# Kernel optimization log

Hardware: AMD Instinct MI355X
Metric: run time of the kernel (lower is better)

Reference implementation:

```python
import jax, jax.numpy as jnp
import numpy as np

N, E, D, H, C = 100000, 1600000, 128, 128, 47
EPS = 1e-5


def setup_inputs() -> dict:
    key = jax.random.key(0)
    ks = jax.random.split(key, 10)
    s = 1.0 / np.sqrt(D).astype(np.float32)
    return {
        "x": jax.random.normal(ks[0], (N, D), jnp.float32),
        "edge_index": jax.random.randint(ks[1], (2, E), 0, N, jnp.int32),
        "Wl0": jax.random.normal(ks[2], (H, D), jnp.float32) * s,
        "bl0": jnp.zeros((H,), jnp.float32),
        "Wr0": jax.random.normal(ks[3], (H, D), jnp.float32) * s,
        "g0": jnp.ones((H,), jnp.float32),
        "b0": jnp.zeros((H,), jnp.float32),
        "Wl1": jax.random.normal(ks[4], (H, H), jnp.float32) * s,
        "bl1": jnp.zeros((H,), jnp.float32),
        "Wr1": jax.random.normal(ks[5], (H, H), jnp.float32) * s,
        "g1": jnp.ones((H,), jnp.float32),
        "b1": jnp.zeros((H,), jnp.float32),
        "Wl2": jax.random.normal(ks[6], (C, H), jnp.float32) * s,
        "bl2": jnp.zeros((C,), jnp.float32),
        "Wr2": jax.random.normal(ks[7], (C, H), jnp.float32) * s,
    }


def _sage_conv(x, edge_index, Wl, bl, Wr):
    # PyG SAGEConv(mean aggr): out = lin_l(mean_{j in N(i)} x_j) + lin_r(x_i)
    dst, src = edge_index[0], edge_index[1]
    n = x.shape[0]
    msg = x[src]                                             # [E, d] gather
    summed = jax.ops.segment_sum(msg, dst, num_segments=n)   # [N, d] scatter-add
    deg = jax.ops.segment_sum(jnp.ones((msg.shape[0],), x.dtype), dst, num_segments=n)
    agg = summed / jnp.maximum(deg, 1.0)[:, None]            # mean over neighbors
    return agg @ Wl.T + bl + x @ Wr.T


def _bn(x, g, b):
    # BatchNorm1d, training-mode batch statistics (biased variance)
    mu = jnp.mean(x, axis=0)
    var = jnp.mean(jnp.square(x - mu), axis=0)
    return (x - mu) * jax.lax.rsqrt(var + EPS) * g + b


def reference(x, edge_index, Wl0, bl0, Wr0, g0, b0, Wl1, bl1, Wr1, g1, b1, Wl2, bl2, Wr2):
    h = _sage_conv(x, edge_index, Wl0, bl0, Wr0)
    h = jax.nn.relu(_bn(h, g0, b0))          # dropout treated as identity (deterministic reference)
    h = _sage_conv(h, edge_index, Wl1, bl1, Wr1)
    h = jax.nn.relu(_bn(h, g1, b1))
    return _sage_conv(h, edge_index, Wl2, bl2, Wr2)
```

## Files before the change

### kernel.cpp

```cpp
#include <hip/hip_runtime.h>

typedef __attribute__((ext_vector_type(8))) short short8;
typedef __attribute__((ext_vector_type(4))) float f32x4;

constexpr float BN_EPS = 1e-5f;
#define NBUCKETS 128
#define SLOT 24576

__device__ __forceinline__ ushort f2bf(float f) {
  uint u = __float_as_uint(f);
  u = (u + 0x7fffu + ((u >> 16) & 1u)) >> 16;
  return (ushort)u;
}
__device__ __forceinline__ float bf2f(ushort h) { return __uint_as_float((uint)h << 16); }
__device__ __forceinline__ float bf2f_lo(uint v) { return __uint_as_float(v << 16); }
__device__ __forceinline__ float bf2f_hi(uint v) { return __uint_as_float(v & 0xffff0000u); }

typedef __attribute__((address_space(1))) const unsigned int* as1_cu32;
typedef __attribute__((address_space(3))) unsigned int* as3_u32;
__device__ __forceinline__ void gload_lds16(const void* g, void* l) {
  __builtin_amdgcn_global_load_lds((as1_cu32)g, (as3_u32)l, 16, 0, 0);
}


__global__ __launch_bounds__(256) void k_prep(const int* __restrict__ dst, const int* __restrict__ src, int E,
                                              int* __restrict__ bcur, uint* __restrict__ ebuf,
                                              const float* __restrict__ x, ushort* __restrict__ Xb, int n4,
                                              const float* __restrict__ Wl0, const float* __restrict__ Wr0,
                                              const float* __restrict__ Wl1, const float* __restrict__ Wr1,
                                              const float* __restrict__ Wl2, const float* __restrict__ Wr2,
                                              ushort* __restrict__ W0l, ushort* __restrict__ W0r,
                                              ushort* __restrict__ W1l, ushort* __restrict__ W1r,
                                              ushort* __restrict__ Wc, float* __restrict__ statsAll,
                                              int C, int binGrid, int castGrid) {
  int bb = blockIdx.x;
  if (bb < binGrid) {
    __shared__ int h[NBUCKETS];
    __shared__ int base[NBUCKETS];
    __shared__ int cur[NBUCKETS];
    const int e0 = bb * 8192;
    const int e1 = min(e0 + 8192, E);
    for (int i = threadIdx.x; i < NBUCKETS; i += 256) h[i] = 0;
    __syncthreads();
    for (int e = e0 + threadIdx.x * 4; e < e1; e += 1024) {
      int4 d = *reinterpret_cast<const int4*>(&dst[e]);
      if (e + 3 < e1) {
        atomicAdd(&h[d.x >> 10], 1); atomicAdd(&h[d.y >> 10], 1);
        atomicAdd(&h[d.z >> 10], 1); atomicAdd(&h[d.w >> 10], 1);
      } else {
        for (int j = 0; e + j < e1; ++j) atomicAdd(&h[dst[e + j] >> 10], 1);
      }
    }
    __syncthreads();
    if (threadIdx.x < NBUCKETS) {
      base[threadIdx.x] = threadIdx.x * SLOT + atomicAdd(&bcur[threadIdx.x], h[threadIdx.x]);
      cur[threadIdx.x] = 0;
    }
    __syncthreads();
    for (int e = e0 + threadIdx.x * 4; e < e1; e += 1024) {
      int4 d = *reinterpret_cast<const int4*>(&dst[e]);
      int4 s = *reinterpret_cast<const int4*>(&src[e]);
      int dd[4] = {d.x, d.y, d.z, d.w};
      int ss[4] = {s.x, s.y, s.z, s.w};
      for (int j = 0; j < 4 && e + j < e1; ++j) {
        int b = dd[j] >> 10;
        int pos = base[b] + atomicAdd(&cur[b], 1);
        ebuf[pos] = (uint)(dd[j] & 1023) | ((uint)ss[j] << 10);
      }
    }
    return;
  }
  bb -= binGrid;
  if (bb < 64) {
    const float* s = (bb < 16) ? Wl0 : (bb < 32) ? Wr0 : (bb < 48) ? Wl1 : Wr1;
    ushort* d = (bb < 16) ? W0l : (bb < 32) ? W0r : (bb < 48) ? W1l : W1r;
    int i = (bb & 15) * 256 + threadIdx.x;
    float4 v = reinterpret_cast<const float4*>(s)[i];
    ushort4 o;
    o.x = f2bf(v.x); o.y = f2bf(v.y); o.z = f2bf(v.z); o.w = f2bf(v.w);
    reinterpret_cast<ushort4*>(d)[i] = o;
    return;
  }
  bb -= 64;
  if (bb < 64) {
    int i = bb * 256 + threadIdx.x;
    int r = i >> 7, k = i & 127;
    float v = 0.f;
    if (r < C) v = Wl2[r * 128 + k];
    else if (r >= 64 && r < 64 + C) v = Wr2[(r - 64) * 128 + k];
    Wc[i] = f2bf(v);
    return;
  }
  bb -= 64;
  if (bb < castGrid) {
    for (int i = bb * 256 + threadIdx.x; i < n4; i += castGrid * 256) {
      float4 v = reinterpret_cast<const float4*>(x)[i];
      ushort4 o;
      o.x = f2bf(v.x); o.y = f2bf(v.y); o.z = f2bf(v.z); o.w = f2bf(v.w);
      reinterpret_cast<ushort4*>(Xb)[i] = o;
    }
    return;
  }
  for (int i = threadIdx.x; i < 512; i += 256) statsAll[i] = 0.f;
}

__global__ __launch_bounds__(512) void k_bucket_build(const uint* __restrict__ ebuf, const int* __restrict__ bend,
                                                      int* __restrict__ rp, int* __restrict__ deg,
                                                      float* __restrict__ deg_inv, int* __restrict__ csr, int N) {
  __shared__ int cnt[1024];
  __shared__ int pre[1024];
  __shared__ int tmp[1024];
  const int blk = blockIdx.x, tid = threadIdx.x;
  const int base = blk << 10;
  const int p0 = blk * SLOT, p1 = p0 + bend[blk];
  for (int i = tid; i < 1024; i += 512) cnt[i] = 0;
  __syncthreads();
  for (int p = p0 + tid; p < p1; p += 512) atomicAdd(&cnt[ebuf[p] & 1023u], 1);
  __syncthreads();
  for (int i = tid; i < 1024; i += 512) pre[i] = cnt[i];
  __syncthreads();
  for (int off = 1; off < 1024; off <<= 1) {
    for (int i = tid; i < 1024; i += 512) tmp[i] = (i >= off) ? pre[i - off] : 0;
    __syncthreads();
    for (int i = tid; i < 1024; i += 512) pre[i] += tmp[i];
    __syncthreads();
  }
  for (int i = tid; i < 1024; i += 512) {
    int node = base + i;
    if (node < N) {
      int c = cnt[i];
      rp[node] = p0 + pre[i] - c;
      deg[node] = c;
      deg_inv[node] = 1.0f / (float)max(c, 1);
    }
    tmp[i] = pre[i] - cnt[i];
  }
  __syncthreads();
  for (int p = p0 + tid; p < p1; p += 512) {
    uint pr = ebuf[p];
    int pos = p0 + atomicAdd(&tmp[pr & 1023u], 1);
    csr[pos] = (int)(pr >> 10);
  }
}


template <bool PRE_BN>
__global__ __launch_bounds__(512, 4) void k_fused(const ushort* __restrict__ X, const ushort* __restrict__ Bsrc,
                                                  const ushort* __restrict__ WA, const ushort* __restrict__ WB,
                                                  const int* __restrict__ rp, const int* __restrict__ deg,
                                                  const float* __restrict__ deg_inv, const int* __restrict__ csr,
                                                  const float* __restrict__ sums, const float* __restrict__ gw,
                                                  const float* __restrict__ bw, float invM,
                                                  float* __restrict__ partial, ushort* __restrict__ Z, int M) {
  __shared__ ushort sA[64 * 128];
  __shared__ ushort sB[64 * 128];
  __shared__ float red[2][4][128];
  __shared__ float ssc[PRE_BN ? 128 : 1];
  __shared__ float ssh[PRE_BN ? 128 : 1];
  const int tid = threadIdx.x;
  const int wave = tid >> 6, lane = tid & 63;
  const int rfrag = lane & 15, kgrp = lane >> 4;
  const int li = rfrag;
  const int row0 = blockIdx.x * 64;

  if (PRE_BN && tid < 128) {
    float mean = sums[tid] * invM;
    float var = fmaxf(sums[128 + tid] * invM - mean * mean, 0.f);
    float sc = gw[tid] * rsqrtf(var + BN_EPS);
    ssc[tid] = sc;
    ssh[tid] = fmaf(-mean, sc, bw[tid]);
  }

#pragma unroll
  for (int i = 0; i < 2; ++i) {
    int c = wave * 2 + i;
    int lb = c * 1024 + lane * 16;
    int row = lb >> 8, bin = lb & 255;
    int gr = min(row0 + row, M - 1);
    int sb = bin ^ ((row & 7) << 4);
    gload_lds16((const char*)Bsrc + (size_t)gr * 256 + sb, (char*)sB + c * 1024);
  }

  float scr[8], shr[8];
  if (PRE_BN) {
#pragma unroll
    for (int e = 0; e < 8; ++e) {
      int f = li * 8 + e;
      float mean = sums[f] * invM;
      float var = fmaxf(sums[128 + f] * invM - mean * mean, 0.f);
      scr[e] = gw[f] * rsqrtf(var + BN_EPS);
      shr[e] = fmaf(-mean, scr[e], bw[f]);
    }
  }

#define BN8(vv, A0, A1, e0)                                                     \
  {                                                                             \
    float xl = bf2f_lo(vv), xh = bf2f_hi(vv);                                   \
    if (PRE_BN) {                                                               \
      xl = fmaxf(fmaf(xl, scr[e0], shr[e0]), 0.f);                              \
      xh = fmaxf(fmaf(xh, scr[e0 + 1], shr[e0 + 1]), 0.f);                      \
    }                                                                           \
    A0 += xl; A1 += xh;                                                         \
  }

  const uint4* X16 = reinterpret_cast<const uint4*>(X);
#pragma unroll
  for (int g = 0; g < 2; ++g) {
    const int lrow = wave * 8 + g * 4 + kgrp;
    const int node = row0 + lrow;
    float a0 = 0.f, a1 = 0.f, a2 = 0.f, a3 = 0.f, a4 = 0.f, a5 = 0.f, a6 = 0.f, a7 = 0.f;
    if (node < M) {
      const int start = rp[node];
      const int c = deg[node];
      int p = 0;
      for (; p + 7 < c; p += 8) {
        int idx[8];
#pragma unroll
        for (int u = 0; u < 8; ++u) idx[u] = csr[start + p + u];
        uint4 v[8];
#pragma unroll
        for (int u = 0; u < 8; ++u) v[u] = X16[(size_t)idx[u] * 16 + li];
#pragma unroll
        for (int u = 0; u < 8; ++u) {
          BN8(v[u].x, a0, a1, 0); BN8(v[u].y, a2, a3, 2);
          BN8(v[u].z, a4, a5, 4); BN8(v[u].w, a6, a7, 6);
        }
      }
      if (p + 3 < c) {
        int idx[4];
#pragma unroll
        for (int u = 0; u < 4; ++u) idx[u] = csr[start + p + u];
        uint4 v[4];
#pragma unroll
        for (int u = 0; u < 4; ++u) v[u] = X16[(size_t)idx[u] * 16 + li];
#pragma unroll
        for (int u = 0; u < 4; ++u) {
          BN8(v[u].x, a0, a1, 0); BN8(v[u].y, a2, a3, 2);
          BN8(v[u].z, a4, a5, 4); BN8(v[u].w, a6, a7, 6);
        }
        p += 4;
      }
      for (; p < c; ++p) {
        uint4 v = X16[(size_t)csr[start + p] * 16 + li];
        BN8(v.x, a0, a1, 0); BN8(v.y, a2, a3, 2);
        BN8(v.z, a4, a5, 4); BN8(v.w, a6, a7, 6);
      }
      const float di = deg_inv[node];
      a0 *= di; a1 *= di; a2 *= di; a3 *= di;
      a4 *= di; a5 *= di; a6 *= di; a7 *= di;
    }
    uint4 o;
    o.x = (uint)f2bf(a0) | ((uint)f2bf(a1) << 16);
    o.y = (uint)f2bf(a2) | ((uint)f2bf(a3) << 16);
    o.z = (uint)f2bf(a4) | ((uint)f2bf(a5) << 16);
    o.w = (uint)f2bf(a6) | ((uint)f2bf(a7) << 16);
    *reinterpret_cast<uint4*>((char*)sA + lrow * 256 + ((li * 16) ^ ((lrow & 7) << 4))) = o;
  }
#undef BN8

  short8 wfA[4], wfB[4];
  {
    const ushort* wa = WA + (wave * 16 + rfrag) * 128 + kgrp * 8;
    const ushort* wb = WB + (wave * 16 + rfrag) * 128 + kgrp * 8;
#pragma unroll
    for (int s = 0; s < 4; ++s) {
      wfA[s] = *reinterpret_cast<const short8*>(wa + s * 32);
      wfB[s] = *reinterpret_cast<const short8*>(wb + s * 32);
    }
  }
  __syncthreads();

  if (PRE_BN) {
#pragma unroll
    for (int i = 0; i < 2; ++i) {
      int addr = (wave * 2 + i) * 1024 + lane * 16;
      int row = addr >> 8, bin = addr & 255;
      int col0 = (bin ^ ((row & 7) << 4)) >> 1;
      uint4 v = *reinterpret_cast<const uint4*>((const char*)sB + addr);
      uint vv[4] = {v.x, v.y, v.z, v.w};
      uint ov[4];
#pragma unroll
      for (int q = 0; q < 4; ++q) {
        int f = col0 + q * 2;
        float xl = fmaxf(fmaf(bf2f_lo(vv[q]), ssc[f], ssh[f]), 0.f);
        float xh = fmaxf(fmaf(bf2f_hi(vv[q]), ssc[f + 1], ssh[f + 1]), 0.f);
        ov[q] = (uint)f2bf(xl) | ((uint)f2bf(xh) << 16);
      }
      *reinterpret_cast<uint4*>((char*)sB + addr) = make_uint4(ov[0], ov[1], ov[2], ov[3]);
    }
    __syncthreads();
  }

  f32x4 acc[4];
#pragma unroll
  for (int i = 0; i < 4; ++i) acc[i] = (f32x4){0.f, 0.f, 0.f, 0.f};

  const int rs = (rfrag & 7) << 4;
#pragma unroll
  for (int strip = 0; strip < 4; ++strip) {
    const int r = strip * 16 + rfrag;
    short8 af[4], bf[4];
#pragma unroll
    for (int s = 0; s < 4; ++s) {
      int off = (kgrp * 16 + s * 64) ^ rs;
      af[s] = *reinterpret_cast<const short8*>((const char*)sA + r * 256 + off);
      bf[s] = *reinterpret_cast<const short8*>((const char*)sB + r * 256 + off);
    }
#pragma unroll
    for (int s = 0; s < 4; ++s)
      acc[strip] = __builtin_amdgcn_mfma_f32_16x16x32_bf16(af[s], wfA[s], acc[strip], 0, 0, 0);
#pragma unroll
    for (int s = 0; s < 4; ++s)
      acc[strip] = __builtin_amdgcn_mfma_f32_16x16x32_bf16(bf[s], wfB[s], acc[strip], 0, 0, 0);
  }

  {
    float s1 = 0.f, s2 = 0.f;
#pragma unroll
    for (int strip = 0; strip < 4; ++strip) {
#pragma unroll
      for (int rr = 0; rr < 4; ++rr) {
        int grow = row0 + strip * 16 + kgrp * 4 + rr;
        if (grow < M) {
          float v = acc[strip][rr];
          s1 += v;
          s2 = fmaf(v, v, s2);
        }
      }
    }
    s1 += __shfl_xor(s1, 16); s2 += __shfl_xor(s2, 16);
    s1 += __shfl_xor(s1, 32); s2 += __shfl_xor(s2, 32);
    if (kgrp == 0) {
      partial[(size_t)blockIdx.x * 256 + wave * 16 + rfrag] = s1;
      partial[(size_t)blockIdx.x * 256 + 128 + wave * 16 + rfrag] = s2;
    }
  }
  __syncthreads();

  const int cb = (wave * 16 + rfrag) * 2;
#pragma unroll
  for (int strip = 0; strip < 4; ++strip) {
#pragma unroll
    for (int rr = 0; rr < 4; ++rr) {
      int row = strip * 16 + kgrp * 4 + rr;
      *reinterpret_cast<ushort*>((char*)sA + row * 256 + (cb ^ ((row & 7) << 4))) = f2bf(acc[strip][rr]);
    }
  }
  __syncthreads();

#pragma unroll
  for (int i = 0; i < 2; ++i) {
    int lb = (wave * 2 + i) * 1024 + lane * 16;
    int row = lb >> 8, bin = lb & 255;
    int gr = row0 + row;
    if (gr < M)
      *reinterpret_cast<uint4*>((char*)Z + (size_t)gr * 256 + bin) =
          *reinterpret_cast<const uint4*>((const char*)sA + row * 256 + (bin ^ ((row & 7) << 4)));
  }
}


__global__ __launch_bounds__(256) void k_bn_reduce(const float* __restrict__ partial, int nblk,
                                                   float* __restrict__ stats) {
  float acc = 0.f;
  for (int b = blockIdx.x; b < nblk; b += gridDim.x) acc += partial[(size_t)b * 256 + threadIdx.x];
  atomicAdd(&stats[threadIdx.x], acc);
}


__global__ __launch_bounds__(512, 6) void k_gemm1(const ushort* __restrict__ H, const ushort* __restrict__ Wc,
                                                  const float* __restrict__ sums, const float* __restrict__ gw,
                                                  const float* __restrict__ bw, float invM,
                                                  ushort* __restrict__ Yb, ushort* __restrict__ Rb, int M) {
  __shared__ ushort sA[64 * 128];
  __shared__ float ssc[128];
  __shared__ float ssh[128];
  const int tid = threadIdx.x;
  const int wave = tid >> 6, lane = tid & 63;
  const int rfrag = lane & 15, kgrp = lane >> 4;
  const int row0 = blockIdx.x * 64;

  if (tid < 128) {
    float mean = sums[tid] * invM;
    float var = fmaxf(sums[128 + tid] * invM - mean * mean, 0.f);
    float sc = gw[tid] * rsqrtf(var + BN_EPS);
    ssc[tid] = sc;
    ssh[tid] = fmaf(-mean, sc, bw[tid]);
  }

#pragma unroll
  for (int i = 0; i < 2; ++i) {
    int c = wave * 2 + i;
    int lb = c * 1024 + lane * 16;
    int row = lb >> 8, bin = lb & 255;
    int gr = min(row0 + row, M - 1);
    int sb = bin ^ ((row & 7) << 4);
    gload_lds16((const char*)H + (size_t)gr * 256 + sb, (char*)sA + c * 1024);
  }

  short8 wf[4];
  {
    const ushort* wp = Wc + (wave * 16 + rfrag) * 128 + kgrp * 8;
#pragma unroll
    for (int s = 0; s < 4; ++s) wf[s] = *reinterpret_cast<const short8*>(wp + s * 32);
  }
  __syncthreads();

#pragma unroll
  for (int i = 0; i < 2; ++i) {
    int addr = (wave * 2 + i) * 1024 + lane * 16;
    int row = addr >> 8, bin = addr & 255;
    int col0 = (bin ^ ((row & 7) << 4)) >> 1;
    uint4 v = *reinterpret_cast<const uint4*>((const char*)sA + addr);
    uint vv[4] = {v.x, v.y, v.z, v.w};
    uint ov[4];
#pragma unroll
    for (int q = 0; q < 4; ++q) {
      int f = col0 + q * 2;
      float xl = fmaxf(fmaf(bf2f_lo(vv[q]), ssc[f], ssh[f]), 0.f);
      float xh = fmaxf(fmaf(bf2f_hi(vv[q]), ssc[f + 1], ssh[f + 1]), 0.f);
      ov[q] = (uint)f2bf(xl) | ((uint)f2bf(xh) << 16);
    }
    *reinterpret_cast<uint4*>((char*)sA + addr) = make_uint4(ov[0], ov[1], ov[2], ov[3]);
  }
  __syncthreads();

  f32x4 acc[4];
#pragma unroll
  for (int i = 0; i < 4; ++i) acc[i] = (f32x4){0.f, 0.f, 0.f, 0.f};
  const int rs = (rfrag & 7) << 4;
#pragma unroll
  for (int strip = 0; strip < 4; ++strip) {
    const int r = strip * 16 + rfrag;
    short8 af[4];
#pragma unroll
    for (int s = 0; s < 4; ++s)
      af[s] = *reinterpret_cast<const short8*>((const char*)sA + r * 256 + ((kgrp * 16 + s * 64) ^ rs));
#pragma unroll
    for (int s = 0; s < 4; ++s)
      acc[strip] = __builtin_amdgcn_mfma_f32_16x16x32_bf16(af[s], wf[s], acc[strip], 0, 0, 0);
  }
  __syncthreads();

  const int cb = (wave * 16 + rfrag) * 2;
#pragma unroll
  for (int strip = 0; strip < 4; ++strip) {
#pragma unroll
    for (int rr = 0; rr < 4; ++rr) {
      int row = strip * 16 + kgrp * 4 + rr;
      *reinterpret_cast<ushort*>((char*)sA + row * 256 + (cb ^ ((row & 7) << 4))) = f2bf(acc[strip][rr]);
    }
  }
  __syncthreads();

#pragma unroll
  for (int i = 0; i < 2; ++i) {
    int lb = (wave * 2 + i) * 1024 + lane * 16;
    int row = lb >> 8, bin = lb & 255;
    int gr = row0 + row;
    if (gr < M) {
      uint4 v = *reinterpret_cast<const uint4*>((const char*)sA + row * 256 + (bin ^ ((row & 7) << 4)));
      if (bin < 128) *reinterpret_cast<uint4*>((char*)Yb + (size_t)gr * 128 + bin) = v;
      else *reinterpret_cast<uint4*>((char*)Rb + (size_t)gr * 128 + (bin - 128)) = v;
    }
  }
}


__global__ __launch_bounds__(256) void k_agg47(const ushort* __restrict__ Yb, const ushort* __restrict__ Rb,
                                               const float* __restrict__ bias, const int* __restrict__ rp,
                                               const int* __restrict__ deg, const float* __restrict__ deg_inv,
                                               const int* __restrict__ csr, float* __restrict__ out,
                                               int N, int C) {
  const int wave = threadIdx.x >> 6, lane = threadIdx.x & 63;
  const int sub = lane >> 3, li = lane & 7;
  const int node = blockIdx.x * 32 + wave * 8 + sub;
  if (node >= N) return;
  const int start = rp[node];
  const int c = deg[node];
  const uint4* Y16 = reinterpret_cast<const uint4*>(Yb);
  float a0 = 0.f, a1 = 0.f, a2 = 0.f, a3 = 0.f, a4 = 0.f, a5 = 0.f, a6 = 0.f, a7 = 0.f;
  int p = 0;
  for (; p + 7 < c; p += 8) {
    int idx[8];
#pragma unroll
    for (int u = 0; u < 8; ++u) idx[u] = csr[start + p + u];
    uint4 v[8];
#pragma unroll
    for (int u = 0; u < 8; ++u) v[u] = Y16[(size_t)idx[u] * 8 + li];
#pragma unroll
    for (int u = 0; u < 8; ++u) {
      a0 += bf2f_lo(v[u].x); a1 += bf2f_hi(v[u].x);
      a2 += bf2f_lo(v[u].y); a3 += bf2f_hi(v[u].y);
      a4 += bf2f_lo(v[u].z); a5 += bf2f_hi(v[u].z);
      a6 += bf2f_lo(v[u].w); a7 += bf2f_hi(v[u].w);
    }
  }
  for (; p < c; ++p) {
    uint4 v = Y16[(size_t)csr[start + p] * 8 + li];
    a0 += bf2f_lo(v.x); a1 += bf2f_hi(v.x);
    a2 += bf2f_lo(v.y); a3 += bf2f_hi(v.y);
    a4 += bf2f_lo(v.z); a5 += bf2f_hi(v.z);
    a6 += bf2f_lo(v.w); a7 += bf2f_hi(v.w);
  }
  const float di = deg_inv[node];
  uint4 sv = reinterpret_cast<const uint4*>(Rb)[(size_t)node * 8 + li];
  float s[8] = {bf2f_lo(sv.x), bf2f_hi(sv.x), bf2f_lo(sv.y), bf2f_hi(sv.y),
                bf2f_lo(sv.z), bf2f_hi(sv.z), bf2f_lo(sv.w), bf2f_hi(sv.w)};
  float a[8] = {a0, a1, a2, a3, a4, a5, a6, a7};
#pragma unroll
  for (int j = 0; j < 8; ++j) {
    int f = li * 8 + j;
    if (f < C) out[(size_t)node * C + f] = fmaf(a[j], di, s[j] + bias[f]);
  }
}


extern "C" void kernel_launch(void* const* d_in, const int* in_sizes, int n_in,
                              void* d_out, int out_size, void* d_ws, size_t ws_size,
                              hipStream_t stream) {
  const float* x   = (const float*)d_in[0];
  const int*   ei  = (const int*)d_in[1];
  const float* Wl0 = (const float*)d_in[2];
  const float* Wr0 = (const float*)d_in[4];
  const float* g0  = (const float*)d_in[5];
  const float* b0  = (const float*)d_in[6];
  const float* Wl1 = (const float*)d_in[7];
  const float* Wr1 = (const float*)d_in[9];
  const float* g1  = (const float*)d_in[10];
  const float* b1  = (const float*)d_in[11];
  const float* Wl2 = (const float*)d_in[12];
  const float* bl2 = (const float*)d_in[13];
  const float* Wr2 = (const float*)d_in[14];

  const int N = in_sizes[0] / 128;
  const int E = in_sizes[1] / 2;
  const int C = in_sizes[13];

  const int* edst = ei;
  const int* esrc = ei + E;

  char* w = (char*)d_ws;
  auto al = [](size_t v) { return (v + 255) & ~(size_t)255; };
  size_t off = 0;
  int*    bcur    = (int*)(w + off);    off = al(off + NBUCKETS * 4);
  float*  stats   = (float*)(w + off);  off = al(off + 512 * 4);
  int*    rp      = (int*)(w + off);    off = al(off + (size_t)N * 4);
  int*    deg     = (int*)(w + off);    off = al(off + (size_t)N * 4);
  float*  deg_inv = (float*)(w + off);  off = al(off + (size_t)N * 4);
  int*    csr     = (int*)(w + off);    off = al(off + (size_t)NBUCKETS * SLOT * 4);
  uint*   ebuf    = (uint*)(w + off);   off = al(off + (size_t)NBUCKETS * SLOT * 4);
  ushort* Xb      = (ushort*)(w + off); off = al(off + (size_t)N * 128 * 2);
  ushort* hA      = (ushort*)(w + off); off = al(off + (size_t)N * 128 * 2);
  ushort* hB      = (ushort*)(w + off); off = al(off + (size_t)N * 128 * 2);
  ushort* W0l     = (ushort*)(w + off); off = al(off + 16384 * 2);
  ushort* W0r     = (ushort*)(w + off); off = al(off + 16384 * 2);
  ushort* W1l     = (ushort*)(w + off); off = al(off + 16384 * 2);
  ushort* W1r     = (ushort*)(w + off); off = al(off + 16384 * 2);
  ushort* Wc      = (ushort*)(w + off); off = al(off + 16384 * 2);
  const int nblkG = (N + 63) / 64;
  float*  partial = (float*)(w + off);  off = al(off + (size_t)nblkG * 256 * 4);

  float* stats0 = stats;
  float* stats1 = stats + 256;
  ushort* Yb = hB;
  ushort* Rb = hB + (size_t)N * 64;

  const int binGrid = (E + 8191) / 8192;
  const int castGrid = 384;
  const int nbBuck = (N + 1023) / 1024;
  const int agg47Grid = (N + 31) / 32;
  const float invM = 1.0f / (float)N;

  hipMemsetAsync(bcur, 0, NBUCKETS * 4, stream);

  k_prep<<<binGrid + 128 + castGrid + 1, 256, 0, stream>>>(
      edst, esrc, E, bcur, ebuf, x, Xb, N * 32,
      Wl0, Wr0, Wl1, Wr1, Wl2, Wr2, W0l, W0r, W1l, W1r, Wc, stats, C, binGrid, castGrid);

  k_bucket_build<<<nbBuck, 512, 0, stream>>>(ebuf, bcur, rp, deg, deg_inv, csr, N);

  k_fused<false><<<nblkG, 512, 0, stream>>>(Xb, Xb, W0l, W0r, rp, deg, deg_inv, csr,
                                            nullptr, nullptr, nullptr, 0.f, partial, hB, N);
  k_bn_reduce<<<64, 256, 0, stream>>>(partial, nblkG, stats0);

  k_fused<true><<<nblkG, 512, 0, stream>>>(hB, hB, W1l, W1r, rp, deg, deg_inv, csr,
                                           stats0, g0, b0, invM, partial, hA, N);
  k_bn_reduce<<<64, 256, 0, stream>>>(partial, nblkG, stats1);

  k_gemm1<<<nblkG, 512, 0, stream>>>(hA, Wc, stats1, g1, b1, invM, Yb, Rb, N);
  k_agg47<<<agg47Grid, 256, 0, stream>>>(Yb, Rb, bl2, rp, deg, deg_inv, csr, (float*)d_out, N, C);
}
```

Measured before the change: 344.4 us.

## Apply layer-0 BN+ReLU once in a standalone pass instead of per gathered neighbor

Layer 1 used to apply BN+ReLU to every gathered neighbor row inside the mean-aggregation loop, which repeats that work about once per incoming edge. This change adds a separate elementwise kernel that normalizes the layer-0 output in place, so a single non-templated fused kernel can do a plain gather-sum for both layers. It also prefetches the next eight CSR indices while the current neighbor rows are being accumulated. The cost is an extra kernel launch and a full read and write of the hidden activations. BN output is also now rounded to bf16 before aggregation, which slightly changes numerics.

```diff
diff --git a/kernel.cpp b/kernel.cpp
--- a/kernel.cpp
+++ b/kernel.cpp
@@ -144,32 +144,18 @@
 }
 
 
-template <bool PRE_BN>
 __global__ __launch_bounds__(512, 4) void k_fused(const ushort* __restrict__ X, const ushort* __restrict__ Bsrc,
                                                   const ushort* __restrict__ WA, const ushort* __restrict__ WB,
                                                   const int* __restrict__ rp, const int* __restrict__ deg,
                                                   const float* __restrict__ deg_inv, const int* __restrict__ csr,
-                                                  const float* __restrict__ sums, const float* __restrict__ gw,
-                                                  const float* __restrict__ bw, float invM,
                                                   float* __restrict__ partial, ushort* __restrict__ Z, int M) {
   __shared__ ushort sA[64 * 128];
   __shared__ ushort sB[64 * 128];
-  __shared__ float red[2][4][128];
-  __shared__ float ssc[PRE_BN ? 128 : 1];
-  __shared__ float ssh[PRE_BN ? 128 : 1];
   const int tid = threadIdx.x;
   const int wave = tid >> 6, lane = tid & 63;
   const int rfrag = lane & 15, kgrp = lane >> 4;
   const int li = rfrag;
   const int row0 = blockIdx.x * 64;
-
-  if (PRE_BN && tid < 128) {
-    float mean = sums[tid] * invM;
-    float var = fmaxf(sums[128 + tid] * invM - mean * mean, 0.f);
-    float sc = gw[tid] * rsqrtf(var + BN_EPS);
-    ssc[tid] = sc;
-    ssh[tid] = fmaf(-mean, sc, bw[tid]);
-  }
 
 #pragma unroll
   for (int i = 0; i < 2; ++i) {
@@ -179,28 +165,6 @@
     int gr = min(row0 + row, M - 1);
     int sb = bin ^ ((row & 7) << 4);
     gload_lds16((const char*)Bsrc + (size_t)gr * 256 + sb, (char*)sB + c * 1024);
-  }
-
-  float scr[8], shr[8];
-  if (PRE_BN) {
-#pragma unroll
-    for (int e = 0; e < 8; ++e) {
-      int f = li * 8 + e;
-      float mean = sums[f] * invM;
-      float var = fmaxf(sums[128 + f] * invM - mean * mean, 0.f);
-      scr[e] = gw[f] * rsqrtf(var + BN_EPS);
-      shr[e] = fmaf(-mean, scr[e], bw[f]);
-    }
-  }
-
-#define BN8(vv, A0, A1, e0)                                                     \
-  {                                                                             \
-    float xl = bf2f_lo(vv), xh = bf2f_hi(vv);                                   \
-    if (PRE_BN) {                                                               \
-      xl = fmaxf(fmaf(xl, scr[e0], shr[e0]), 0.f);                              \
-      xh = fmaxf(fmaf(xh, scr[e0 + 1], shr[e0 + 1]), 0.f);                      \
-    }                                                                           \
-    A0 += xl; A1 += xh;                                                         \
   }
 
   const uint4* X16 = reinterpret_cast<const uint4*>(X);
@@ -213,17 +177,28 @@
       const int start = rp[node];
       const int c = deg[node];
       int p = 0;
-      for (; p + 7 < c; p += 8) {
+      if (c >= 8) {
         int idx[8];
 #pragma unroll
-        for (int u = 0; u < 8; ++u) idx[u] = csr[start + p + u];
-        uint4 v[8];
-#pragma unroll
-        for (int u = 0; u < 8; ++u) v[u] = X16[(size_t)idx[u] * 16 + li];
-#pragma unroll
-        for (int u = 0; u < 8; ++u) {
-          BN8(v[u].x, a0, a1, 0); BN8(v[u].y, a2, a3, 2);
-          BN8(v[u].z, a4, a5, 4); BN8(v[u].w, a6, a7, 6);
+        for (int u = 0; u < 8; ++u) idx[u] = csr[start + u];
+        while (true) {
+          uint4 v[8];
+#pragma unroll
+          for (int u = 0; u < 8; ++u) v[u] = X16[(size_t)idx[u] * 16 + li];
+          p += 8;
+          const bool more = (p + 7 < c);
+          if (more) {
+#pragma unroll
+            for (int u = 0; u < 8; ++u) idx[u] = csr[start + p + u];
+          }
+#pragma unroll
+          for (int u = 0; u < 8; ++u) {
+            a0 += bf2f_lo(v[u].x); a1 += bf2f_hi(v[u].x);
+            a2 += bf2f_lo(v[u].y); a3 += bf2f_hi(v[u].y);
+            a4 += bf2f_lo(v[u].z); a5 += bf2f_hi(v[u].z);
+            a6 += bf2f_lo(v[u].w); a7 += bf2f_hi(v[u].w);
+          }
+          if (!more) break;
         }
       }
       if (p + 3 < c) {
@@ -235,15 +210,19 @@
         for (int u = 0; u < 4; ++u) v[u] = X16[(size_t)idx[u] * 16 + li];
 #pragma unroll
         for (int u = 0; u < 4; ++u) {
-          BN8(v[u].x, a0, a1, 0); BN8(v[u].y, a2, a3, 2);
-          BN8(v[u].z, a4, a5, 4); BN8(v[u].w, a6, a7, 6);
+          a0 += bf2f_lo(v[u].x); a1 += bf2f_hi(v[u].x);
+          a2 += bf2f_lo(v[u].y); a3 += bf2f_hi(v[u].y);
+          a4 += bf2f_lo(v[u].z); a5 += bf2f_hi(v[u].z);
+          a6 += bf2f_lo(v[u].w); a7 += bf2f_hi(v[u].w);
         }
         p += 4;
       }
       for (; p < c; ++p) {
         uint4 v = X16[(size_t)csr[start + p] * 16 + li];
-        BN8(v.x, a0, a1, 0); BN8(v.y, a2, a3, 2);
-        BN8(v.z, a4, a5, 4); BN8(v.w, a6, a7, 6);
+        a0 += bf2f_lo(v.x); a1 += bf2f_hi(v.x);
+        a2 += bf2f_lo(v.y); a3 += bf2f_hi(v.y);
+        a4 += bf2f_lo(v.z); a5 += bf2f_hi(v.z);
+        a6 += bf2f_lo(v.w); a7 += bf2f_hi(v.w);
       }
       const float di = deg_inv[node];
       a0 *= di; a1 *= di; a2 *= di; a3 *= di;
@@ -256,7 +235,6 @@
     o.w = (uint)f2bf(a6) | ((uint)f2bf(a7) << 16);
     *reinterpret_cast<uint4*>((char*)sA + lrow * 256 + ((li * 16) ^ ((lrow & 7) << 4))) = o;
   }
-#undef BN8
 
   short8 wfA[4], wfB[4];
   {
@@ -269,27 +247,6 @@
     }
   }
   __syncthreads();
-
-  if (PRE_BN) {
-#pragma unroll
-    for (int i = 0; i < 2; ++i) {
-      int addr = (wave * 2 + i) * 1024 + lane * 16;
-      int row = addr >> 8, bin = addr & 255;
-      int col0 = (bin ^ ((row & 7) << 4)) >> 1;
-      uint4 v = *reinterpret_cast<const uint4*>((const char*)sB + addr);
-      uint vv[4] = {v.x, v.y, v.z, v.w};
-      uint ov[4];
-#pragma unroll
-      for (int q = 0; q < 4; ++q) {
-        int f = col0 + q * 2;
-        float xl = fmaxf(fmaf(bf2f_lo(vv[q]), ssc[f], ssh[f]), 0.f);
-        float xh = fmaxf(fmaf(bf2f_hi(vv[q]), ssc[f + 1], ssh[f + 1]), 0.f);
-        ov[q] = (uint)f2bf(xl) | ((uint)f2bf(xh) << 16);
-      }
-      *reinterpret_cast<uint4*>((char*)sB + addr) = make_uint4(ov[0], ov[1], ov[2], ov[3]);
-    }
-    __syncthreads();
-  }
 
   f32x4 acc[4];
 #pragma unroll
@@ -365,6 +322,33 @@
   float acc = 0.f;
   for (int b = blockIdx.x; b < nblk; b += gridDim.x) acc += partial[(size_t)b * 256 + threadIdx.x];
   atomicAdd(&stats[threadIdx.x], acc);
+}
+
+
+__global__ __launch_bounds__(256) void k_bn_relu(uint2* __restrict__ Z, int n2, const float* __restrict__ sums,
+                                                 const float* __restrict__ g, const float* __restrict__ b,
+                                                 float invM) {
+  __shared__ float ss[256];
+  if (threadIdx.x < 128) {
+    int f = threadIdx.x;
+    float mean = sums[f] * invM;
+    float var = fmaxf(sums[128 + f] * invM - mean * mean, 0.f);
+    float sc = g[f] * rsqrtf(var + BN_EPS);
+    ss[f] = sc;
+    ss[128 + f] = fmaf(-mean, sc, b[f]);
+  }
+  __syncthreads();
+  for (int i = blockIdx.x * 256 + threadIdx.x; i < n2; i += gridDim.x * 256) {
+    uint2 v = Z[i];
+    int f0 = (i & 31) * 4;
+    float a0 = fmaxf(fmaf(bf2f_lo(v.x), ss[f0 + 0], ss[128 + f0 + 0]), 0.f);
+    float a1 = fmaxf(fmaf(bf2f_hi(v.x), ss[f0 + 1], ss[128 + f0 + 1]), 0.f);
+    float a2 = fmaxf(fmaf(bf2f_lo(v.y), ss[f0 + 2], ss[128 + f0 + 2]), 0.f);
+    float a3 = fmaxf(fmaf(bf2f_hi(v.y), ss[f0 + 3], ss[128 + f0 + 3]), 0.f);
+    v.x = (uint)f2bf(a0) | ((uint)f2bf(a1) << 16);
+    v.y = (uint)f2bf(a2) | ((uint)f2bf(a3) << 16);
+    Z[i] = v;
+  }
 }
 
 
@@ -580,12 +564,12 @@
 
   k_bucket_build<<<nbBuck, 512, 0, stream>>>(ebuf, bcur, rp, deg, deg_inv, csr, N);
 
-  k_fused<false><<<nblkG, 512, 0, stream>>>(Xb, Xb, W0l, W0r, rp, deg, deg_inv, csr,
-                                            nullptr, nullptr, nullptr, 0.f, partial, hB, N);
+  k_fused<<<nblkG, 512, 0, stream>>>(Xb, Xb, W0l, W0r, rp, deg, deg_inv, csr, partial, hB, N);
   k_bn_reduce<<<64, 256, 0, stream>>>(partial, nblkG, stats0);
 
-  k_fused<true><<<nblkG, 512, 0, stream>>>(hB, hB, W1l, W1r, rp, deg, deg_inv, csr,
-                                           stats0, g0, b0, invM, partial, hA, N);
+  k_bn_relu<<<2048, 256, 0, stream>>>((uint2*)hB, N * 32, stats0, g0, b0, invM);
+
+  k_fused<<<nblkG, 512, 0, stream>>>(hB, hB, W1l, W1r, rp, deg, deg_inv, csr, partial, hA, N);
   k_bn_reduce<<<64, 256, 0, stream>>>(partial, nblkG, stats1);
 
   k_gemm1<<<nblkG, 512, 0, stream>>>(hA, Wc, stats1, g1, b1, invM, Yb, Rb, N);
```

Result: faster. 303.5 us, median of 2 (-11.9%).
